# Performance work log

Hardware: AMD Instinct MI355X
Metric: run time of the kernel (lower is better)

The kernel has to match this reference:

```python
import jax, jax.numpy as jnp
import numpy as np

D_IN = 1024
D_PROJ = 128
B = 65536


def setup_inputs() -> dict:
    key = jax.random.key(0)
    k1, k2, kw, kb = jax.random.split(key, 4)
    x1 = jax.random.normal(k1, (B, D_IN), dtype=jnp.float32)
    x2 = jax.random.normal(k2, (B, D_IN), dtype=jnp.float32)
    # nn.Linear default init: U(-1/sqrt(fan_in), 1/sqrt(fan_in))
    bound = 1.0 / np.sqrt(D_IN)
    W = jax.random.uniform(kw, (D_PROJ, D_IN), dtype=jnp.float32, minval=-bound, maxval=bound)
    b = jax.random.uniform(kb, (D_PROJ,), dtype=jnp.float32, minval=-bound, maxval=bound)
    return {"x1": x1, "x2": x2, "W": W, "b": b}


def reference(x1, x2, W, b):
    # forward_one: Linear(1024->128) + Tanh  (shared weights for both branches)
    o1 = jnp.tanh(x1 @ W.T + b)  # [B, 128]
    o2 = jnp.tanh(x2 @ W.T + b)  # [B, 128]
    # torch.diag(o1 @ o2.T) == row-wise dot product; compute it directly.
    sim = jnp.sum(o1 * o2, axis=-1)  # [B]
    return jax.nn.sigmoid(sim)
```

## Files before the change

### kernel.cpp

```cpp
#include <hip/hip_runtime.h>
#include <hip/hip_bf16.h>

typedef _Float16 half8 __attribute__((ext_vector_type(8)));
typedef float float4v __attribute__((ext_vector_type(4)));

#define D_IN 1024
#define D_PROJ 128
#define KSTEPS 32
#define CTILES 8

__global__ __launch_bounds__(256) void wconv_kernel(const float* __restrict__ W,
                                                    _Float16* __restrict__ wf) {
    int t = blockIdx.x * 256 + threadIdx.x;
    int l  = t & 63;
    int ct = (t >> 6) & 7;
    int ks = t >> 9;
    const float* src = W + (size_t)(ct * 16 + (l & 15)) * D_IN + ks * 32 + ((l >> 4) * 8);
    float4v lo = *reinterpret_cast<const float4v*>(src);
    float4v hi = *reinterpret_cast<const float4v*>(src + 4);
    half8 h;
#pragma unroll
    for (int j = 0; j < 4; ++j) {
        h[j]     = (_Float16)lo[j];
        h[j + 4] = (_Float16)hi[j];
    }
    *reinterpret_cast<half8*>(wf + (size_t)t * 8) = h;
}

__device__ __forceinline__ float fast_tanh(float x) {
    float e = __builtin_amdgcn_exp2f(x * 2.885390081777927f);
    return 1.0f - 2.0f / (e + 1.0f);
}

__global__ __launch_bounds__(256) void fused_kernel(const float* __restrict__ x1,
                                                    const float* __restrict__ x2,
                                                    const _Float16* __restrict__ wf,
                                                    const float* __restrict__ b,
                                                    float* __restrict__ out) {
    const int l    = threadIdx.x & 63;
    const int wave = threadIdx.x >> 6;
    const int rowBase = blockIdx.x * 64 + wave * 16;
    const int lr = l & 15;
    const int lg = l >> 4;

    const float4v* p1 = reinterpret_cast<const float4v*>(
        x1 + (size_t)(rowBase + lr) * D_IN + lg * 8);
    const float4v* p2 = reinterpret_cast<const float4v*>(
        x2 + (size_t)(rowBase + lr) * D_IN + lg * 8);
    const half8* wfrag = reinterpret_cast<const half8*>(wf) + l;

    float4v acc1[CTILES], acc2[CTILES];
#pragma unroll
    for (int ct = 0; ct < CTILES; ++ct) {
        acc1[ct] = (float4v){0.f, 0.f, 0.f, 0.f};
        acc2[ct] = (float4v){0.f, 0.f, 0.f, 0.f};
    }

#pragma unroll 2
    for (int ks = 0; ks < KSTEPS; ++ks) {
        float4v a1lo = __builtin_nontemporal_load(p1 + ks * 8);
        float4v a1hi = __builtin_nontemporal_load(p1 + ks * 8 + 1);
        float4v a2lo = __builtin_nontemporal_load(p2 + ks * 8);
        float4v a2hi = __builtin_nontemporal_load(p2 + ks * 8 + 1);
        half8 a1, a2;
#pragma unroll
        for (int j = 0; j < 4; ++j) {
            a1[j]     = (_Float16)a1lo[j];
            a1[j + 4] = (_Float16)a1hi[j];
            a2[j]     = (_Float16)a2lo[j];
            a2[j + 4] = (_Float16)a2hi[j];
        }
        const half8* wp = wfrag + (size_t)ks * 8 * 64;
#pragma unroll
        for (int ct = 0; ct < CTILES; ++ct) {
            half8 bw = wp[ct * 64];
            acc1[ct] = __builtin_amdgcn_mfma_f32_16x16x32_f16(a1, bw, acc1[ct], 0, 0, 0);
            acc2[ct] = __builtin_amdgcn_mfma_f32_16x16x32_f16(a2, bw, acc2[ct], 0, 0, 0);
        }
    }

    float bias[CTILES];
#pragma unroll
    for (int ct = 0; ct < CTILES; ++ct) bias[ct] = b[ct * 16 + lr];

    float s[4] = {0.f, 0.f, 0.f, 0.f};
#pragma unroll
    for (int ct = 0; ct < CTILES; ++ct) {
#pragma unroll
        for (int r = 0; r < 4; ++r) {
            float t1 = fast_tanh(acc1[ct][r] + bias[ct]);
            float t2 = fast_tanh(acc2[ct][r] + bias[ct]);
            s[r] += t1 * t2;
        }
    }
#pragma unroll
    for (int r = 0; r < 4; ++r) {
        float v = s[r];
        v += __shfl_xor(v, 1);
        v += __shfl_xor(v, 2);
        v += __shfl_xor(v, 4);
        v += __shfl_xor(v, 8);
        if (lr == 0) {
            int row = rowBase + lg * 4 + r;
            float e = __builtin_amdgcn_exp2f(-v * 1.4426950408889634f);
            out[row] = 1.0f / (1.0f + e);
        }
    }
}

extern "C" void kernel_launch(void* const* d_in, const int* in_sizes, int n_in,
                              void* d_out, int out_size, void* d_ws, size_t ws_size,
                              hipStream_t stream) {
    const float* x1 = (const float*)d_in[0];
    const float* x2 = (const float*)d_in[1];
    const float* W  = (const float*)d_in[2];
    const float* b  = (const float*)d_in[3];
    float* out = (float*)d_out;
    _Float16* wf = (_Float16*)d_ws;

    hipLaunchKernelGGL(wconv_kernel, dim3(64), dim3(256), 0, stream, W, wf);
    hipLaunchKernelGGL(fused_kernel, dim3(1024), dim3(256), 0, stream,
                       x1, x2, wf, b, out);
}
```

Baseline: 608.2 us.

## Stage x tiles through LDS with coalesced loads and register prefetch

Activations are now loaded with fully coalesced 512-byte row segments, converted to fp16 and written to per-wave padded LDS buffers, then reloaded in the MFMA fragment layout. The next phase's global loads are issued before the LDS writes, giving software prefetch, and launch bounds request two blocks per CU. The aim is better DRAM coalescing and latency hiding on a bandwidth-bound stream of x1/x2. The cost is extra LDS traffic, higher register pressure and a lgkmcnt wait each phase; only a waitcnt, not a barrier, orders the per-wave LDS writes and reads.

Measured after the change: 567.3 us. 6.7% less time.

```diff
diff --git a/kernel.cpp b/kernel.cpp
--- a/kernel.cpp
+++ b/kernel.cpp
@@ -2,12 +2,16 @@
 #include <hip/hip_bf16.h>
 
 typedef _Float16 half8 __attribute__((ext_vector_type(8)));
+typedef _Float16 half4 __attribute__((ext_vector_type(4)));
 typedef float float4v __attribute__((ext_vector_type(4)));
 
 #define D_IN 1024
 #define D_PROJ 128
-#define KSTEPS 32
 #define CTILES 8
+#define NPH 8
+#define SLOTS 8
+#define ROWSTRIDE 272
+#define WAVE_LDS (2 * 16 * ROWSTRIDE)
 
 __global__ __launch_bounds__(256) void wconv_kernel(const float* __restrict__ W,
                                                     _Float16* __restrict__ wf) {
@@ -32,21 +36,25 @@
     return 1.0f - 2.0f / (e + 1.0f);
 }
 
-__global__ __launch_bounds__(256) void fused_kernel(const float* __restrict__ x1,
-                                                    const float* __restrict__ x2,
-                                                    const _Float16* __restrict__ wf,
-                                                    const float* __restrict__ b,
-                                                    float* __restrict__ out) {
+__global__ __launch_bounds__(256, 2) void fused_kernel(const float* __restrict__ x1,
+                                                       const float* __restrict__ x2,
+                                                       const _Float16* __restrict__ wf,
+                                                       const float* __restrict__ b,
+                                                       float* __restrict__ out) {
+    __shared__ __align__(16) char smem[4 * WAVE_LDS];
+
     const int l    = threadIdx.x & 63;
     const int wave = threadIdx.x >> 6;
     const int rowBase = blockIdx.x * 64 + wave * 16;
     const int lr = l & 15;
     const int lg = l >> 4;
 
-    const float4v* p1 = reinterpret_cast<const float4v*>(
-        x1 + (size_t)(rowBase + lr) * D_IN + lg * 8);
-    const float4v* p2 = reinterpret_cast<const float4v*>(
-        x2 + (size_t)(rowBase + lr) * D_IN + lg * 8);
+    char* ldsA = smem + wave * WAVE_LDS;
+    char* ldsB = ldsA + 16 * ROWSTRIDE;
+
+    const char* g1 = (const char*)x1 + (((size_t)(rowBase + (l >> 5))) << 12) + ((l & 31) << 4);
+    const char* g2 = (const char*)x2 + (((size_t)(rowBase + (l >> 5))) << 12) + ((l & 31) << 4);
+
     const half8* wfrag = reinterpret_cast<const half8*>(wf) + l;
 
     float4v acc1[CTILES], acc2[CTILES];
@@ -56,26 +64,52 @@
         acc2[ct] = (float4v){0.f, 0.f, 0.f, 0.f};
     }
 
-#pragma unroll 2
-    for (int ks = 0; ks < KSTEPS; ++ks) {
-        float4v a1lo = __builtin_nontemporal_load(p1 + ks * 8);
-        float4v a1hi = __builtin_nontemporal_load(p1 + ks * 8 + 1);
-        float4v a2lo = __builtin_nontemporal_load(p2 + ks * 8);
-        float4v a2hi = __builtin_nontemporal_load(p2 + ks * 8 + 1);
-        half8 a1, a2;
+    float4v P1[SLOTS], P2[SLOTS];
 #pragma unroll
-        for (int j = 0; j < 4; ++j) {
-            a1[j]     = (_Float16)a1lo[j];
-            a1[j + 4] = (_Float16)a1hi[j];
-            a2[j]     = (_Float16)a2lo[j];
-            a2[j + 4] = (_Float16)a2hi[j];
+    for (int i = 0; i < SLOTS; ++i) {
+        P1[i] = *reinterpret_cast<const float4v*>(g1 + i * 8192);
+        P2[i] = *reinterpret_cast<const float4v*>(g2 + i * 8192);
+    }
+
+    const int woff = (l >> 5) * ROWSTRIDE + (l & 31) * 8;
+
+#pragma unroll
+    for (int ph = 0; ph < NPH; ++ph) {
+        half4 h1[SLOTS], h2[SLOTS];
+#pragma unroll
+        for (int i = 0; i < SLOTS; ++i) {
+#pragma unroll
+            for (int j = 0; j < 4; ++j) {
+                h1[i][j] = (_Float16)P1[i][j];
+                h2[i][j] = (_Float16)P2[i][j];
+            }
         }
-        const half8* wp = wfrag + (size_t)ks * 8 * 64;
+        if (ph + 1 < NPH) {
 #pragma unroll
-        for (int ct = 0; ct < CTILES; ++ct) {
-            half8 bw = wp[ct * 64];
-            acc1[ct] = __builtin_amdgcn_mfma_f32_16x16x32_f16(a1, bw, acc1[ct], 0, 0, 0);
-            acc2[ct] = __builtin_amdgcn_mfma_f32_16x16x32_f16(a2, bw, acc2[ct], 0, 0, 0);
+            for (int i = 0; i < SLOTS; ++i) {
+                P1[i] = *reinterpret_cast<const float4v*>(g1 + (ph + 1) * 512 + i * 8192);
+                P2[i] = *reinterpret_cast<const float4v*>(g2 + (ph + 1) * 512 + i * 8192);
+            }
+        }
+#pragma unroll
+        for (int i = 0; i < SLOTS; ++i) {
+            *reinterpret_cast<half4*>(ldsA + 2 * i * ROWSTRIDE + woff) = h1[i];
+            *reinterpret_cast<half4*>(ldsB + 2 * i * ROWSTRIDE + woff) = h2[i];
+        }
+        asm volatile("s_waitcnt lgkmcnt(0)" ::: "memory");
+        __builtin_amdgcn_sched_barrier(0);
+
+#pragma unroll
+        for (int ks = 0; ks < 4; ++ks) {
+            half8 a1 = *reinterpret_cast<const half8*>(ldsA + lr * ROWSTRIDE + ks * 64 + lg * 16);
+            half8 a2 = *reinterpret_cast<const half8*>(ldsB + lr * ROWSTRIDE + ks * 64 + lg * 16);
+            const half8* wp = wfrag + (size_t)(ph * 4 + ks) * 8 * 64;
+#pragma unroll
+            for (int ct = 0; ct < CTILES; ++ct) {
+                half8 bw = wp[ct * 64];
+                acc1[ct] = __builtin_amdgcn_mfma_f32_16x16x32_f16(a1, bw, acc1[ct], 0, 0, 0);
+                acc2[ct] = __builtin_amdgcn_mfma_f32_16x16x32_f16(a2, bw, acc2[ct], 0, 0, 0);
+            }
         }
     }
 
```
